# Kernel optimization log

Hardware: AMD Instinct MI355X
Metric: run time of the kernel (lower is better)

Reference implementation:

```python
import jax, jax.numpy as jnp
import numpy as np

ROUTING_ITERS = 3
EPS = 1e-9


def squash(s, axis=-1):
    sq_norm = jnp.sum(s * s, axis=axis, keepdims=True)
    scale = sq_norm / (1.0 + sq_norm)
    return scale * s / jnp.sqrt(sq_norm + EPS)


def setup_inputs() -> dict:
    key = jax.random.key(0)
    k_u, k_w = jax.random.split(key)
    B, P, C, OUT, IN = 256, 2048, 10, 16, 8
    u = jax.random.normal(k_u, (B, P, IN), dtype=jnp.float32)
    W = 0.01 * jax.random.normal(k_w, (1, P, C, OUT, IN), dtype=jnp.float32)
    return {"u": u, "W": W}


def reference(u, W):
    # u: [B, P, IN], W: [1, P, C, OUT, IN]
    # u_hat[b,p,c,o] = sum_i W[0,p,c,o,i] * u[b,p,i]
    u_hat = jnp.einsum('pcoi,bpi->bpco', W[0], u)  # [B, P, C, OUT]
    B, P, C, _ = u_hat.shape
    b = jnp.zeros((B, P, C), dtype=u_hat.dtype)
    v = None
    for _ in range(ROUTING_ITERS):
        c = jax.nn.softmax(b, axis=2)                     # [B, P, C]
        s = jnp.einsum('bpc,bpco->bco', c, u_hat)         # [B, C, OUT]
        v = squash(s, axis=-1)                            # [B, C, OUT]
        b = b + jnp.einsum('bpco,bco->bpc', u_hat, v)     # agreement update
    return v
```

## Files before the change

kernel.cpp:

```cpp
#include <hip/hip_runtime.h>
#include <hip/hip_fp16.h>


#define Bn 256
#define Pn 2048
#define Cn 10
#define On 16
#define In 8
#define ROW 160
#define BT 64
#define PPB 16
#define NPT (Pn / PPB)
#define TPB 256
#define GRID ((Bn / BT) * NPT)

typedef _Float16 f16x8 __attribute__((ext_vector_type(8)));
typedef _Float16 h2f __attribute__((ext_vector_type(2)));
typedef float f32x4 __attribute__((ext_vector_type(4)));

__device__ __forceinline__ void gl_lds16(const void* g, void* l) {
  __builtin_amdgcn_global_load_lds(
      (const __attribute__((address_space(1))) unsigned int*)g,
      (__attribute__((address_space(3))) unsigned int*)l, 16, 0, 0);
}

__device__ __forceinline__ h2f pack2(float a, float b) {
  __half2 t = __floats2half2_rn(a, b);
  return *reinterpret_cast<h2f*>(&t);
}

__global__ __launch_bounds__(256) void k_prepw(const float* __restrict__ W,
                                               _Float16* __restrict__ Wh) {
  const size_t base = (size_t)blockIdx.x * 1280;
#pragma unroll
  for (int r = 0; r < 5; ++r) {
    const int i = threadIdx.x + 256 * r;
    Wh[base + i] = (_Float16)W[base + i];
  }
}

__global__ __launch_bounds__(256) void k_prepu(const float* __restrict__ u,
                                               _Float16* __restrict__ uT) {
  const int p = blockIdx.x;
  const int b = threadIdx.x;
  const float4* src = reinterpret_cast<const float4*>(u + ((size_t)b * Pn + p) * In);
  const float4 a = src[0], c = src[1];
  f16x8 o;
  o[0] = (_Float16)a.x; o[1] = (_Float16)a.y; o[2] = (_Float16)a.z; o[3] = (_Float16)a.w;
  o[4] = (_Float16)c.x; o[5] = (_Float16)c.y; o[6] = (_Float16)c.z; o[7] = (_Float16)c.w;
  *reinterpret_cast<f16x8*>(uT + ((size_t)p * Bn + b) * In) = o;
}

template <int MODE>
__global__ __launch_bounds__(TPB, 2) void k_cap(const _Float16* __restrict__ uT,
                                                const _Float16* __restrict__ Wh,
                                                const float* __restrict__ s1,
                                                const float* __restrict__ s2,
                                                float* __restrict__ part) {
  __shared__ _Float16 wH[PPB * 1280];
  const int x = blockIdx.x;
  const int bt = x >> 7;
  const int pt = x & 127;
  const int tid = threadIdx.x;
  const int w = tid >> 6;
  const int lane = tid & 63;
  const int col = lane & 15;
  const int quad = lane >> 4;
  const int b = bt * BT + w * 16 + col;
  const int p0 = pt * PPB;

  {
    const char* src = reinterpret_cast<const char*>(Wh + (size_t)p0 * 1280);
    char* dst = reinterpret_cast<char*>(wH);
#pragma unroll
    for (int r = 0; r < 10; ++r)
      gl_lds16(src + r * 4096 + tid * 16, dst + r * 4096 + tid * 16);
  }

  h2f vh[Cn][2];
  if (MODE >= 1) {
    const float4* spA = reinterpret_cast<const float4*>(s1 + (size_t)b * ROW);
    const float4* spB = reinterpret_cast<const float4*>(s2 + (size_t)b * ROW);
#pragma unroll
    for (int c = 0; c < Cn; ++c) {
      const float4 a0 = spA[c * 4 + 0], a1 = spA[c * 4 + 1];
      const float4 a2 = spA[c * 4 + 2], a3 = spA[c * 4 + 3];
      float sqA = a0.x * a0.x + a0.y * a0.y + a0.z * a0.z + a0.w * a0.w;
      sqA += a1.x * a1.x + a1.y * a1.y + a1.z * a1.z + a1.w * a1.w;
      sqA += a2.x * a2.x + a2.y * a2.y + a2.z * a2.z + a2.w * a2.w;
      sqA += a3.x * a3.x + a3.y * a3.y + a3.z * a3.z + a3.w * a3.w;
      sqA *= 0.01f;
      const float facA = 0.1f * (sqA / (1.f + sqA)) / sqrtf(sqA + 1e-9f);
      const float4 qa = spA[c * 4 + quad];
      float v0 = facA * qa.x, v1_ = facA * qa.y;
      float v2_ = facA * qa.z, v3_ = facA * qa.w;
      if (MODE == 2) {
        const float4 b0 = spB[c * 4 + 0], b1 = spB[c * 4 + 1];
        const float4 b2 = spB[c * 4 + 2], b3 = spB[c * 4 + 3];
        float sqB = b0.x * b0.x + b0.y * b0.y + b0.z * b0.z + b0.w * b0.w;
        sqB += b1.x * b1.x + b1.y * b1.y + b1.z * b1.z + b1.w * b1.w;
        sqB += b2.x * b2.x + b2.y * b2.y + b2.z * b2.z + b2.w * b2.w;
        sqB += b3.x * b3.x + b3.y * b3.y + b3.z * b3.z + b3.w * b3.w;
        const float facB = (sqB / (1.f + sqB)) / sqrtf(sqB + 1e-9f);
        const float4 qb = spB[c * 4 + quad];
        v0 += facB * qb.x; v1_ += facB * qb.y;
        v2_ += facB * qb.z; v3_ += facB * qb.w;
      }
      vh[c][0] = pack2(v0, v1_);
      vh[c][1] = pack2(v2_, v3_);
    }
  }

  f32x4 acc[Cn];
  const f32x4 zc = {0.f, 0.f, 0.f, 0.f};
#pragma unroll
  for (int c = 0; c < Cn; ++c) acc[c] = zc;

  const _Float16* urow = uT + ((size_t)p0 * Bn + b) * In;
  f16x8 uf = *reinterpret_cast<const f16x8*>(urow);
  const f16x8 zb = {0, 0, 0, 0, 0, 0, 0, 0};
  const bool isq0 = (quad == 0);

  __syncthreads();

  for (int ip = 0; ip < PPB; ++ip) {
    f16x8 ufn = uf;
    if (ip + 1 < PPB)
      ufn = *reinterpret_cast<const f16x8*>(urow + (size_t)(ip + 1) * Bn * In);
    const f16x8 ub = isq0 ? uf : zb;
    const _Float16* wp = wH + ip * 1280 + col * 8;

    if (MODE == 0) {
#pragma unroll
      for (int c = 0; c < Cn; ++c) {
        const f16x8 aW = *reinterpret_cast<const f16x8*>(wp + c * 128);
        acc[c] = __builtin_amdgcn_mfma_f32_16x16x32_f16(aW, ub, acc[c], 0, 0, 0);
      }
    } else {
      float lf[Cn];
      h2f uhh[Cn][2];
#pragma unroll
      for (int c = 0; c < Cn; ++c) {
        const f16x8 aW = *reinterpret_cast<const f16x8*>(wp + c * 128);
        const f32x4 uh =
            __builtin_amdgcn_mfma_f32_16x16x32_f16(aW, ub, zc, 0, 0, 0);
        float lp = uh[0] * (float)vh[c][0][0];
        lp = __builtin_fmaf(uh[1], (float)vh[c][0][1], lp);
        lp = __builtin_fmaf(uh[2], (float)vh[c][1][0], lp);
        lp = __builtin_fmaf(uh[3], (float)vh[c][1][1], lp);
        lf[c] = lp;
        uhh[c][0] = pack2(uh[0], uh[1]);
        uhh[c][1] = pack2(uh[2], uh[3]);
      }
#pragma unroll
      for (int c = 0; c < Cn; ++c) {
        lf[c] += __shfl_xor(lf[c], 16, 64);
        lf[c] += __shfl_xor(lf[c], 32, 64);
      }
      float m = lf[0];
#pragma unroll
      for (int c = 1; c < Cn; ++c) m = fmaxf(m, lf[c]);
      float ss = 0.f;
#pragma unroll
      for (int c = 0; c < Cn; ++c) {
        lf[c] = __expf(lf[c] - m);
        ss += lf[c];
      }
      const float inv = 1.f / ss;
#pragma unroll
      for (int c = 0; c < Cn; ++c) {
        const float cv = lf[c] * inv;
        acc[c][0] = __builtin_fmaf(cv, (float)uhh[c][0][0], acc[c][0]);
        acc[c][1] = __builtin_fmaf(cv, (float)uhh[c][0][1], acc[c][1]);
        acc[c][2] = __builtin_fmaf(cv, (float)uhh[c][1][0], acc[c][2]);
        acc[c][3] = __builtin_fmaf(cv, (float)uhh[c][1][1], acc[c][3]);
      }
    }
    uf = ufn;
  }

  float* pb = part + ((size_t)x * BT + w * 16 + col) * ROW;
#pragma unroll
  for (int c = 0; c < Cn; ++c)
    *reinterpret_cast<f32x4*>(pb + c * 16 + quad * 4) = acc[c];
}

__global__ __launch_bounds__(256) void k_red(const float* __restrict__ part,
                                             float* __restrict__ s) {
  const int cell = blockIdx.x * 256 + threadIdx.x;
  const int b = cell / 160, rem = cell - 160 * b;
  const int bt = b >> 6, bl = b & 63;
  const float* p0 = part + ((size_t)(bt * NPT) * BT + bl) * ROW + rem;
  float a0 = 0.f, a1 = 0.f, a2 = 0.f, a3 = 0.f;
  float a4 = 0.f, a5 = 0.f, a6 = 0.f, a7 = 0.f;
#pragma unroll 4
  for (int pt = 0; pt < NPT; pt += 8) {
    a0 += p0[(size_t)(pt + 0) * BT * ROW];
    a1 += p0[(size_t)(pt + 1) * BT * ROW];
    a2 += p0[(size_t)(pt + 2) * BT * ROW];
    a3 += p0[(size_t)(pt + 3) * BT * ROW];
    a4 += p0[(size_t)(pt + 4) * BT * ROW];
    a5 += p0[(size_t)(pt + 5) * BT * ROW];
    a6 += p0[(size_t)(pt + 6) * BT * ROW];
    a7 += p0[(size_t)(pt + 7) * BT * ROW];
  }
  s[cell] = ((a0 + a1) + (a2 + a3)) + ((a4 + a5) + (a6 + a7));
}

__global__ __launch_bounds__(256) void k_out(const float* __restrict__ s,
                                             float* __restrict__ out) {
  const int gi = blockIdx.x * 256 + threadIdx.x;
  const int b = gi / 10, c = gi - 10 * b;
  const float* sp = s + (size_t)b * ROW + c * 16;
  float sq = 0.f;
#pragma unroll
  for (int o = 0; o < On; ++o) { const float xx = sp[o]; sq += xx * xx; }
  const float fac = (sq / (1.f + sq)) / sqrtf(sq + 1e-9f);
  float* op = out + (size_t)b * ROW + c * 16;
#pragma unroll
  for (int o = 0; o < On; ++o) op[o] = fac * sp[o];
}

extern "C" void kernel_launch(void* const* d_in, const int* in_sizes, int n_in,
                              void* d_out, int out_size, void* d_ws, size_t ws_size,
                              hipStream_t stream) {
  (void)in_sizes; (void)n_in; (void)out_size;
  const float* u = (const float*)d_in[0];
  const float* W = (const float*)d_in[1];
  float* out = (float*)d_out;
  float* s1 = (float*)d_ws;
  float* s2 = s1 + (size_t)Bn * ROW;
  float* s3 = s2 + (size_t)Bn * ROW;
  float* part = s3 + (size_t)Bn * ROW;
  _Float16* Wh = (_Float16*)(part + (size_t)GRID * BT * ROW);
  _Float16* uTp = Wh + (size_t)Pn * Cn * On * In;
  const size_t need =
      ((size_t)3 * Bn * ROW + (size_t)GRID * BT * ROW) * sizeof(float) +
      ((size_t)Pn * Cn * On * In + (size_t)Pn * Bn * In) * sizeof(_Float16);
  if (ws_size < need) return;
  k_prepw<<<Pn, 256, 0, stream>>>(W, Wh);
  k_prepu<<<Pn, 256, 0, stream>>>(u, uTp);
  k_cap<0><<<GRID, TPB, 0, stream>>>(uTp, Wh, s1, s1, part);
  k_red<<<160, 256, 0, stream>>>(part, s1);
  k_cap<1><<<GRID, TPB, 0, stream>>>(uTp, Wh, s1, s1, part);
  k_red<<<160, 256, 0, stream>>>(part, s2);
  k_cap<2><<<GRID, TPB, 0, stream>>>(uTp, Wh, s1, s2, part);
  k_red<<<160, 256, 0, stream>>>(part, s3);
  k_out<<<10, 256, 0, stream>>>(s3, out);
}
```

Measured before the change: 204.6 us.

## Split capsule point loop across two wave groups and parallelize partial reduction

Doubles k_cap block size so two groups of four waves each process half of the 16 points, combining their accumulators through LDS before writing partials. The partial reduction kernel is split into four chunks per cell that accumulate with atomicAdd into zeroed buffers, and the u transpose kernel handles two points per block. This shortens the serial per-thread loop and raises reduction parallelism, at the cost of an extra barrier/LDS pass, a memset, and nondeterministic float summation order.

```diff
diff --git a/kernel.cpp b/kernel.cpp
--- a/kernel.cpp
+++ b/kernel.cpp
@@ -11,7 +11,7 @@
 #define BT 64
 #define PPB 16
 #define NPT (Pn / PPB)
-#define TPB 256
+#define TPB 512
 #define GRID ((Bn / BT) * NPT)
 
 typedef _Float16 f16x8 __attribute__((ext_vector_type(8)));
@@ -41,14 +41,17 @@
 
 __global__ __launch_bounds__(256) void k_prepu(const float* __restrict__ u,
                                                _Float16* __restrict__ uT) {
-  const int p = blockIdx.x;
+  const int p2 = blockIdx.x * 2;
   const int b = threadIdx.x;
-  const float4* src = reinterpret_cast<const float4*>(u + ((size_t)b * Pn + p) * In);
-  const float4 a = src[0], c = src[1];
-  f16x8 o;
-  o[0] = (_Float16)a.x; o[1] = (_Float16)a.y; o[2] = (_Float16)a.z; o[3] = (_Float16)a.w;
-  o[4] = (_Float16)c.x; o[5] = (_Float16)c.y; o[6] = (_Float16)c.z; o[7] = (_Float16)c.w;
-  *reinterpret_cast<f16x8*>(uT + ((size_t)p * Bn + b) * In) = o;
+  const float4* src = reinterpret_cast<const float4*>(u + ((size_t)b * Pn + p2) * In);
+  const float4 q0 = src[0], q1 = src[1], q2 = src[2], q3 = src[3];
+  f16x8 o0, o1;
+  o0[0] = (_Float16)q0.x; o0[1] = (_Float16)q0.y; o0[2] = (_Float16)q0.z; o0[3] = (_Float16)q0.w;
+  o0[4] = (_Float16)q1.x; o0[5] = (_Float16)q1.y; o0[6] = (_Float16)q1.z; o0[7] = (_Float16)q1.w;
+  o1[0] = (_Float16)q2.x; o1[1] = (_Float16)q2.y; o1[2] = (_Float16)q2.z; o1[3] = (_Float16)q2.w;
+  o1[4] = (_Float16)q3.x; o1[5] = (_Float16)q3.y; o1[6] = (_Float16)q3.z; o1[7] = (_Float16)q3.w;
+  *reinterpret_cast<f16x8*>(uT + ((size_t)p2 * Bn + b) * In) = o0;
+  *reinterpret_cast<f16x8*>(uT + ((size_t)(p2 + 1) * Bn + b) * In) = o1;
 }
 
 template <int MODE>
@@ -57,24 +60,27 @@
                                                 const float* __restrict__ s1,
                                                 const float* __restrict__ s2,
                                                 float* __restrict__ part) {
-  __shared__ _Float16 wH[PPB * 1280];
+  __shared__ float arena[10368];
+  _Float16* wH = reinterpret_cast<_Float16*>(arena);
   const int x = blockIdx.x;
   const int bt = x >> 7;
   const int pt = x & 127;
   const int tid = threadIdx.x;
   const int w = tid >> 6;
+  const int pg = w >> 2;
+  const int wq = w & 3;
   const int lane = tid & 63;
   const int col = lane & 15;
   const int quad = lane >> 4;
-  const int b = bt * BT + w * 16 + col;
+  const int b = bt * BT + wq * 16 + col;
   const int p0 = pt * PPB;
 
   {
     const char* src = reinterpret_cast<const char*>(Wh + (size_t)p0 * 1280);
     char* dst = reinterpret_cast<char*>(wH);
 #pragma unroll
-    for (int r = 0; r < 10; ++r)
-      gl_lds16(src + r * 4096 + tid * 16, dst + r * 4096 + tid * 16);
+    for (int r = 0; r < 5; ++r)
+      gl_lds16(src + r * 8192 + tid * 16, dst + r * 8192 + tid * 16);
   }
 
   h2f vh[Cn][2];
@@ -116,19 +122,19 @@
 #pragma unroll
   for (int c = 0; c < Cn; ++c) acc[c] = zc;
 
-  const _Float16* urow = uT + ((size_t)p0 * Bn + b) * In;
+  const _Float16* urow = uT + ((size_t)(p0 + pg * 8) * Bn + b) * In;
   f16x8 uf = *reinterpret_cast<const f16x8*>(urow);
   const f16x8 zb = {0, 0, 0, 0, 0, 0, 0, 0};
   const bool isq0 = (quad == 0);
 
   __syncthreads();
 
-  for (int ip = 0; ip < PPB; ++ip) {
+  for (int ip = 0; ip < 8; ++ip) {
     f16x8 ufn = uf;
-    if (ip + 1 < PPB)
+    if (ip + 1 < 8)
       ufn = *reinterpret_cast<const f16x8*>(urow + (size_t)(ip + 1) * Bn * In);
     const f16x8 ub = isq0 ? uf : zb;
-    const _Float16* wp = wH + ip * 1280 + col * 8;
+    const _Float16* wp = wH + (pg * 8 + ip) * 1280 + col * 8;
 
     if (MODE == 0) {
 #pragma unroll
@@ -157,9 +163,9 @@
         lf[c] += __shfl_xor(lf[c], 16, 64);
         lf[c] += __shfl_xor(lf[c], 32, 64);
       }
-      float m = lf[0];
-#pragma unroll
-      for (int c = 1; c < Cn; ++c) m = fmaxf(m, lf[c]);
+      float m = fmaxf(fmaxf(__builtin_fmaf(0.f, 0.f, lf[0]), lf[1]), lf[2]);
+      m = fmaxf(m, fmaxf(fmaxf(lf[3], lf[4]), fmaxf(lf[5], lf[6])));
+      m = fmaxf(m, fmaxf(fmaxf(lf[7], lf[8]), lf[9]));
       float ss = 0.f;
 #pragma unroll
       for (int c = 0; c < Cn; ++c) {
@@ -179,22 +185,40 @@
     uf = ufn;
   }
 
-  float* pb = part + ((size_t)x * BT + w * 16 + col) * ROW;
-#pragma unroll
-  for (int c = 0; c < Cn; ++c)
-    *reinterpret_cast<f32x4*>(pb + c * 16 + quad * 4) = acc[c];
+  __syncthreads();
+  float* sAcc = arena;
+  const int row = wq * 16 + col;
+  if (pg == 1) {
+    float* dst = &sAcc[row * 162 + quad * 4];
+#pragma unroll
+    for (int c = 0; c < Cn; ++c)
+      *reinterpret_cast<f32x4*>(dst + c * 16) = acc[c];
+  }
+  __syncthreads();
+  if (pg == 0) {
+    const float* srcp = &sAcc[row * 162 + quad * 4];
+    float* pb = part + ((size_t)x * BT + row) * ROW;
+#pragma unroll
+    for (int c = 0; c < Cn; ++c) {
+      f32x4 t = *reinterpret_cast<const f32x4*>(srcp + c * 16);
+      t = t + acc[c];
+      *reinterpret_cast<f32x4*>(pb + c * 16 + quad * 4) = t;
+    }
+  }
 }
 
 __global__ __launch_bounds__(256) void k_red(const float* __restrict__ part,
                                              float* __restrict__ s) {
   const int cell = blockIdx.x * 256 + threadIdx.x;
+  const int chunk = blockIdx.y;
   const int b = cell / 160, rem = cell - 160 * b;
   const int bt = b >> 6, bl = b & 63;
-  const float* p0 = part + ((size_t)(bt * NPT) * BT + bl) * ROW + rem;
+  const float* p0 =
+      part + ((size_t)(bt * NPT + chunk * 32) * BT + bl) * ROW + rem;
   float a0 = 0.f, a1 = 0.f, a2 = 0.f, a3 = 0.f;
   float a4 = 0.f, a5 = 0.f, a6 = 0.f, a7 = 0.f;
-#pragma unroll 4
-  for (int pt = 0; pt < NPT; pt += 8) {
+#pragma unroll
+  for (int pt = 0; pt < 32; pt += 8) {
     a0 += p0[(size_t)(pt + 0) * BT * ROW];
     a1 += p0[(size_t)(pt + 1) * BT * ROW];
     a2 += p0[(size_t)(pt + 2) * BT * ROW];
@@ -204,7 +228,7 @@
     a6 += p0[(size_t)(pt + 6) * BT * ROW];
     a7 += p0[(size_t)(pt + 7) * BT * ROW];
   }
-  s[cell] = ((a0 + a1) + (a2 + a3)) + ((a4 + a5) + (a6 + a7));
+  atomicAdd(&s[cell], ((a0 + a1) + (a2 + a3)) + ((a4 + a5) + (a6 + a7)));
 }
 
 __global__ __launch_bounds__(256) void k_out(const float* __restrict__ s,
@@ -238,13 +262,14 @@
       ((size_t)3 * Bn * ROW + (size_t)GRID * BT * ROW) * sizeof(float) +
       ((size_t)Pn * Cn * On * In + (size_t)Pn * Bn * In) * sizeof(_Float16);
   if (ws_size < need) return;
+  hipMemsetAsync(s1, 0, (size_t)3 * Bn * ROW * sizeof(float), stream);
   k_prepw<<<Pn, 256, 0, stream>>>(W, Wh);
-  k_prepu<<<Pn, 256, 0, stream>>>(u, uTp);
+  k_prepu<<<Pn / 2, 256, 0, stream>>>(u, uTp);
   k_cap<0><<<GRID, TPB, 0, stream>>>(uTp, Wh, s1, s1, part);
-  k_red<<<160, 256, 0, stream>>>(part, s1);
+  k_red<<<dim3(160, 4), 256, 0, stream>>>(part, s1);
   k_cap<1><<<GRID, TPB, 0, stream>>>(uTp, Wh, s1, s1, part);
-  k_red<<<160, 256, 0, stream>>>(part, s2);
+  k_red<<<dim3(160, 4), 256, 0, stream>>>(part, s2);
   k_cap<2><<<GRID, TPB, 0, stream>>>(uTp, Wh, s1, s2, part);
-  k_red<<<160, 256, 0, stream>>>(part, s3);
+  k_red<<<dim3(160, 4), 256, 0, stream>>>(part, s3);
   k_out<<<10, 256, 0, stream>>>(s3, out);
 }
```

Result: slower. 224.7 us (+9.8%).
